# Kernel tuning notes

Measured on AMD Instinct MI355X. Metric: run time of the kernel, lower is better.

Reference implementation:

```python
import jax, jax.numpy as jnp
import numpy as np

B, L, H, D, M = 4, 2048, 16, 64, 128
EPS = 1e-6


def _create_projection_matrix(key, m, d):
    nb_full_blocks = m // d
    keys = jax.random.split(key, nb_full_blocks + 2)
    blocks = []
    for i in range(nb_full_blocks):
        unstructured = jax.random.normal(keys[i], (d, d), dtype=jnp.float32)
        q, _ = jnp.linalg.qr(unstructured)
        blocks.append(q.T)
    remaining = m - nb_full_blocks * d
    if remaining > 0:
        unstructured = jax.random.normal(keys[nb_full_blocks], (d, d), dtype=jnp.float32)
        q, _ = jnp.linalg.qr(unstructured)
        blocks.append(q.T[:remaining])
    final = jnp.concatenate(blocks, axis=0)  # [m, d]
    multiplier = jnp.linalg.norm(jax.random.normal(keys[-1], (m, d), dtype=jnp.float32), axis=1)
    return multiplier[:, None] * final


def setup_inputs() -> dict:
    key = jax.random.key(0)
    kq, kk, kv, kp = jax.random.split(key, 4)
    return {
        "q": jax.random.normal(kq, (B, L, H, D), dtype=jnp.float32),
        "k": jax.random.normal(kk, (B, L, H, D), dtype=jnp.float32),
        "v": jax.random.normal(kv, (B, L, H, D), dtype=jnp.float32),
        "projection_matrix": _create_projection_matrix(kp, M, D),
    }


def _softmax_kernel(data, proj, is_query, eps=EPS):
    # data: [B,L,H,D], proj: [M,D]
    data = (data.shape[-1] ** -0.25) * data
    ratio = proj.shape[0] ** -0.5
    data_dash = jnp.einsum('blhd,md->blhm', data, proj)  # [B,L,H,M]
    diag = jnp.sum(data * data, axis=-1, keepdims=True) * 0.5  # [B,L,H,1]
    if is_query:
        mx = jnp.max(data_dash, axis=-1, keepdims=True)
    else:
        mx = jnp.max(data_dash, axis=(1, 3), keepdims=True)
    return ratio * (jnp.exp(data_dash - diag - mx) + eps)


def reference(q, k, v, projection_matrix):
    qp = _softmax_kernel(q, projection_matrix, True)   # [B,L,H,M]
    kp = _softmax_kernel(k, projection_matrix, False)  # [B,L,H,M]
    # move L to the front for the causal scan
    qs = jnp.swapaxes(qp, 0, 1)  # [L,B,H,M]
    ks = jnp.swapaxes(kp, 0, 1)  # [L,B,H,M]
    vs = jnp.swapaxes(v, 0, 1)   # [L,B,H,D]

    def step(carry, inp):
        s, dsum = carry                 # s: [B,H,M,D], dsum: [B,H,M]
        q_t, k_t, v_t = inp
        s = s + k_t[..., :, None] * v_t[..., None, :]  # outer product accumulate
        dsum = dsum + k_t
        num = jnp.einsum('bhmd,bhm->bhd', s, q_t)      # [B,H,D]
        den = jnp.einsum('bhm,bhm->bh', q_t, dsum)     # [B,H]
        return (s, dsum), (num, den)

    init = (jnp.zeros((qs.shape[1], qs.shape[2], qs.shape[3], vs.shape[3]), qs.dtype),
            jnp.zeros_like(ks[0]))
    _, (nums, dens) = jax.lax.scan(step, init, (qs, ks, vs))
    av = jnp.swapaxes(nums, 0, 1)          # [B,L,H,D]
    norm = jnp.swapaxes(dens, 0, 1)[..., None]  # [B,L,H,1]
    return av / norm
```

## Files before the change

### kernel.cpp

```cpp
#include <hip/hip_runtime.h>
#include <math.h>

#define B_ 4
#define L_ 2048
#define H_ 16
#define D_ 64
#define M_ 128
#define TC_ 64
#define NC_ (L_ / TC_)
#define EPSK 1e-6f
#define DATA_SCALE 0.35355339059327379f
#define RATIO 0.08838834764831845f

typedef __bf16 bf16;
typedef bf16 bf16x4 __attribute__((ext_vector_type(4)));
typedef bf16 bf16x8 __attribute__((ext_vector_type(8)));
typedef float floatx4 __attribute__((ext_vector_type(4)));

#define PK64 72
#define FS_ 136

__device__ __forceinline__ unsigned pk(bf16 a, bf16 b) {
    return (unsigned)__builtin_bit_cast(unsigned short, a) |
           ((unsigned)__builtin_bit_cast(unsigned short, b) << 16);
}

__device__ __forceinline__ unsigned enc_f(float f) {
    unsigned u = __float_as_uint(f);
    return (u & 0x80000000u) ? ~u : (u | 0x80000000u);
}
__device__ __forceinline__ float dec_f(unsigned u) {
    unsigned b = (u & 0x80000000u) ? (u ^ 0x80000000u) : ~u;
    return __uint_as_float(b);
}

__global__ __launch_bounds__(256) void proj_split(const float* __restrict__ proj,
                                                  bf16* __restrict__ pfh,
                                                  bf16* __restrict__ pfl,
                                                  unsigned* __restrict__ mx) {
    int f = blockIdx.x * 256 + threadIdx.x;
    if (blockIdx.x == 0 && threadIdx.x < B_ * H_) mx[threadIdx.x] = 0u;
    int tc = f >> 7, k0h = (f >> 6) & 1, lane = f & 63;
    int lr = lane & 15, quad = lane >> 4;
    const float* src = proj + (16 * tc + lr) * 64 + k0h * 32 + quad * 8;
    float4 x0 = *(const float4*)src;
    float4 x1 = *(const float4*)(src + 4);
    float a[8] = {x0.x, x0.y, x0.z, x0.w, x1.x, x1.y, x1.z, x1.w};
    bf16x8 hi, lo;
#pragma unroll
    for (int e = 0; e < 8; e++) {
        bf16 h = (bf16)a[e];
        hi[e] = h;
        lo[e] = (bf16)(a[e] - (float)h);
    }
    *(bf16x8*)(pfh + (size_t)f * 8) = hi;
    *(bf16x8*)(pfl + (size_t)f * 8) = lo;
}

__global__ __launch_bounds__(256) void feat_max(const float* __restrict__ k,
                                                const bf16* __restrict__ pfh,
                                                unsigned* __restrict__ mxk) {
    __shared__ float wred[4];
    int tid = threadIdx.x;
    int blk = blockIdx.x;
    int c = blk & 31, h = (blk >> 5) & 15, b = blk >> 9;
    int l0 = c * 64;
    int w = tid >> 6, lane = tid & 63, lr = lane & 15, quad = lane >> 4;

    const float* drow = k +
        ((size_t)(b * L_ + l0 + 16 * w + lr) * H_ + h) * D_ + quad * 8;
    bf16x8 ah[2];
#pragma unroll
    for (int k0 = 0; k0 < 2; k0++) {
        float4 x0 = *(const float4*)(drow + k0 * 32);
        float4 x1 = *(const float4*)(drow + k0 * 32 + 4);
        float a[8] = {x0.x, x0.y, x0.z, x0.w, x1.x, x1.y, x1.z, x1.w};
#pragma unroll
        for (int e = 0; e < 8; e++) ah[k0][e] = (bf16)(DATA_SCALE * a[e]);
    }

    floatx4 acc[8];
#pragma unroll
    for (int tc = 0; tc < 8; tc++) acc[tc] = (floatx4){0.f, 0.f, 0.f, 0.f};
    const bf16x8* ph = (const bf16x8*)pfh + lane;
#pragma unroll
    for (int tc = 0; tc < 8; tc++)
#pragma unroll
        for (int k0 = 0; k0 < 2; k0++) {
            bf16x8 bh = ph[(tc * 2 + k0) * 64];
            acc[tc] = __builtin_amdgcn_mfma_f32_16x16x32_bf16(ah[k0], bh, acc[tc], 0, 0, 0);
        }

    float mm = acc[0][0];
#pragma unroll
    for (int tc = 0; tc < 8; tc++)
#pragma unroll
        for (int reg = 0; reg < 4; reg++) mm = fmaxf(mm, acc[tc][reg]);
#pragma unroll
    for (int off = 1; off < 64; off <<= 1) mm = fmaxf(mm, __shfl_xor(mm, off, 64));
    if (lane == 0) wred[w] = mm;
    __syncthreads();
    if (tid == 0) {
        float g = fmaxf(fmaxf(wred[0], wred[1]), fmaxf(wred[2], wred[3]));
        atomicMax(&mxk[b * H_ + h], enc_f(g));
    }
}

__global__ __launch_bounds__(256) void feat_k(const float* __restrict__ kin,
                                              const bf16* __restrict__ pfh,
                                              const bf16* __restrict__ pfl,
                                              const unsigned* __restrict__ mxk,
                                              bf16* __restrict__ kp) {
    __shared__ __align__(16) bf16 sc[64 * FS_];
    int tid = threadIdx.x;
    int blk = blockIdx.x;
    int c = blk & 31, h = (blk >> 5) & 15, b = blk >> 9;
    int l0 = c * 64;
    int w = tid >> 6, lane = tid & 63, lr = lane & 15, quad = lane >> 4;

    const float* drow = kin +
        ((size_t)(b * L_ + l0 + 16 * w + lr) * H_ + h) * D_ + quad * 8;
    bf16x8 ah[2], al[2];
    float ss = 0.f;
#pragma unroll
    for (int k0 = 0; k0 < 2; k0++) {
        float4 x0 = *(const float4*)(drow + k0 * 32);
        float4 x1 = *(const float4*)(drow + k0 * 32 + 4);
        float a[8] = {x0.x, x0.y, x0.z, x0.w, x1.x, x1.y, x1.z, x1.w};
#pragma unroll
        for (int e = 0; e < 8; e++) {
            float s = DATA_SCALE * a[e];
            ss += s * s;
            bf16 hh = (bf16)s;
            ah[k0][e] = hh;
            al[k0][e] = (bf16)(s - (float)hh);
        }
    }
    ss += __shfl_xor(ss, 16, 64);
    ss += __shfl_xor(ss, 32, 64);
    float ssrow = 0.5f * ss;

    floatx4 acc[8];
#pragma unroll
    for (int tc = 0; tc < 8; tc++) acc[tc] = (floatx4){0.f, 0.f, 0.f, 0.f};
    const bf16x8* ph = (const bf16x8*)pfh + lane;
    const bf16x8* pl = (const bf16x8*)pfl + lane;
#pragma unroll
    for (int tc = 0; tc < 8; tc++)
#pragma unroll
        for (int k0 = 0; k0 < 2; k0++) {
            bf16x8 bh = ph[(tc * 2 + k0) * 64];
            bf16x8 bl = pl[(tc * 2 + k0) * 64];
            acc[tc] = __builtin_amdgcn_mfma_f32_16x16x32_bf16(ah[k0], bh, acc[tc], 0, 0, 0);
            acc[tc] = __builtin_amdgcn_mfma_f32_16x16x32_bf16(al[k0], bh, acc[tc], 0, 0, 0);
            acc[tc] = __builtin_amdgcn_mfma_f32_16x16x32_bf16(ah[k0], bl, acc[tc], 0, 0, 0);
        }

    int t0 = 16 * w + 4 * quad;
    float mxg = dec_f(mxk[b * H_ + h]);
#pragma unroll
    for (int reg = 0; reg < 4; reg++) {
        float dg = __shfl(ssrow, 4 * quad + reg, 64);
        float sh = dg + mxg;
#pragma unroll
        for (int tc = 0; tc < 8; tc++) {
            float val = RATIO * (__expf(acc[tc][reg] - sh) + EPSK);
            sc[(t0 + reg) * FS_ + 16 * tc + lr] = (bf16)val;
        }
    }

    {
        uint4* kout = (uint4*)(kp + (size_t)blk * 8192);
#pragma unroll
        for (int ki = 0; ki < 4; ki++)
            kout[(ki * 4 + w) * 64 + lane] =
                *(const uint4*)(sc + (16 * w + lr) * FS_ + 32 * ki + 8 * quad);
    }
}

__global__ __launch_bounds__(256) void chunk_v(const bf16* __restrict__ kp,
                                               const float* __restrict__ v,
                                               bf16* __restrict__ S,
                                               float* __restrict__ ds,
                                               bf16* __restrict__ vbT) {
    __shared__ __align__(16) bf16 kT[128 * PK64];
    __shared__ __align__(16) bf16 vT[64 * PK64];
    int tid = threadIdx.x;
    int blk = blockIdx.x;
    int c = blk & 31, bh = blk >> 5;
    int h = bh & 15, b = bh >> 4;
    int l0 = c * 64;
    int w = tid >> 6, lane = tid & 63, lr = lane & 15, quad = lane >> 4;

    const bf16* kpt = kp + (size_t)blk * 8192;
#pragma unroll
    for (int i = 0; i < 4; i++) {
        int m8 = w * 4 + i;
        bf16x8 kv = *(const bf16x8*)(kpt +
            (((m8 >> 2) * 4 + (lane >> 4)) * 64 + (m8 & 3) * 16 + (lane & 15)) * 8);
#pragma unroll
        for (int e = 0; e < 8; e++) kT[(m8 * 8 + e) * PK64 + lane] = kv[e];
    }
    {
        const float* vrow = v + ((size_t)(b * L_ + l0 + lane) * H_ + h) * D_;
#pragma unroll
        for (int i = 0; i < 4; i++) {
            int d4 = w * 4 + i;
            float4 x = *(const float4*)(vrow + d4 * 4);
            vT[(d4 * 4 + 0) * PK64 + lane] = (bf16)x.x;
            vT[(d4 * 4 + 1) * PK64 + lane] = (bf16)x.y;
            vT[(d4 * 4 + 2) * PK64 + lane] = (bf16)x.z;
            vT[(d4 * 4 + 3) * PK64 + lane] = (bf16)x.w;
        }
    }
    __syncthreads();

    floatx4 acc[8];
#pragma unroll
    for (int tc = 0; tc < 8; tc++) acc[tc] = (floatx4){0.f, 0.f, 0.f, 0.f};
#pragma unroll
    for (int k0 = 0; k0 < 64; k0 += 32) {
        bf16x8 a = *(const bf16x8*)(vT + (16 * w + lr) * PK64 + k0 + quad * 8);
#pragma unroll
        for (int tc = 0; tc < 8; tc++) {
            bf16x8 bb = *(const bf16x8*)(kT + (16 * tc + lr) * PK64 + k0 + quad * 8);
            acc[tc] = __builtin_amdgcn_mfma_f32_16x16x32_bf16(a, bb, acc[tc], 0, 0, 0);
        }
    }

    {
        size_t ob = (size_t)(bh * D_) * (size_t)L_ + l0;
#pragma unroll
        for (int i = 0; i < 8; i++) {
            int e2 = tid + 256 * i;
            int d = e2 >> 5, tau2 = (e2 & 31) * 2;
            *(unsigned*)(vbT + ob + (size_t)d * L_ + tau2) =
                *(const unsigned*)(vT + d * PK64 + tau2);
        }
    }

    float dsv = 0.f;
    {
        int m = tid >> 1, half = tid & 1;
        const bf16x8* kr = (const bf16x8*)(kT + m * PK64 + half * 32);
#pragma unroll
        for (int j = 0; j < 4; j++) {
            bf16x8 vv = kr[j];
#pragma unroll
            for (int e = 0; e < 8; e++) dsv += (float)vv[e];
        }
        dsv += __shfl_xor(dsv, 1, 64);
    }
    __syncthreads();

    bf16* scr = kT;
#pragma unroll
    for (int tc = 0; tc < 8; tc++)
#pragma unroll
        for (int reg = 0; reg < 4; reg++)
            scr[((tc >> 1) * 4 + w) * 512 +
                (((((tc & 1) << 1) | (lr >> 3)) * 16) + 4 * quad + reg) * 8 +
                (lr & 7)] = (bf16)acc[tc][reg];
    if ((tid & 1) == 0) ds[(size_t)blk * M_ + (tid >> 1)] = dsv;
    __syncthreads();
#pragma unroll
    for (int i = 0; i < 4; i++) {
        int e = tid + 256 * i;
        ((uint4*)S)[(size_t)blk * 1024 + e] = ((const uint4*)scr)[e];
    }
}

__global__ void prefix_SD(unsigned* __restrict__ S, float* __restrict__ ds) {
    int blk = blockIdx.x;
    int seg = blk & 15, bh = blk >> 4;
    int p = seg * 256 + threadIdx.x;
    size_t base = (size_t)bh * NC_ * 4096 + p;
    unsigned uv[NC_];
#pragma unroll
    for (int c = 0; c < NC_; c++) uv[c] = S[base + (size_t)c * 4096];
    float c0 = 0.f, c1 = 0.f;
#pragma unroll
    for (int c = 0; c < NC_; c++) {
        unsigned u = uv[c];
        float f0 = (float)__builtin_bit_cast(bf16, (unsigned short)(u & 0xffffu));
        float f1 = (float)__builtin_bit_cast(bf16, (unsigned short)(u >> 16));
        S[base + (size_t)c * 4096] = pk((bf16)c0, (bf16)c1);
        c0 += f0; c1 += f1;
    }
    if (seg == 0 && threadIdx.x < 128) {
        int m = threadIdx.x;
        size_t dbase = (size_t)bh * NC_ * M_ + m;
        float dv[NC_];
#pragma unroll
        for (int c = 0; c < NC_; c++) dv[c] = ds[dbase + (size_t)c * M_];
        float carry = 0.f;
#pragma unroll
        for (int c = 0; c < NC_; c++) {
            ds[dbase + (size_t)c * M_] = carry;
            carry += dv[c];
        }
    }
}

__global__ __launch_bounds__(256, 4) void attn_q(const float* __restrict__ q,
                                                 const bf16* __restrict__ pfh,
                                                 const bf16* __restrict__ pfl,
                                                 const bf16* __restrict__ kp,
                                                 const bf16* __restrict__ vbT,
                                                 const bf16* __restrict__ Sp,
                                                 const float* __restrict__ dp,
                                                 float* __restrict__ out) {
    __shared__ __align__(16) bf16 fsc[64 * FS_];

    int tid = threadIdx.x;
    int blk = blockIdx.x;
    int c = blk & 31, bh = blk >> 5;
    int h = bh & 15, b = bh >> 4;
    int l0 = c * 64;
    int w = tid >> 6, lane = tid & 63, lr = lane & 15, quad = lane >> 4;

    const float* drow = q +
        ((size_t)(b * L_ + l0 + 16 * w + lr) * H_ + h) * D_ + quad * 8;
    bf16x8 ah[2], al[2];
    float ss = 0.f;
#pragma unroll
    for (int k0 = 0; k0 < 2; k0++) {
        float4 x0 = *(const float4*)(drow + k0 * 32);
        float4 x1 = *(const float4*)(drow + k0 * 32 + 4);
        float a[8] = {x0.x, x0.y, x0.z, x0.w, x1.x, x1.y, x1.z, x1.w};
#pragma unroll
        for (int e = 0; e < 8; e++) {
            float s = DATA_SCALE * a[e];
            ss += s * s;
            bf16 hh = (bf16)s;
            ah[k0][e] = hh;
            al[k0][e] = (bf16)(s - (float)hh);
        }
    }
    ss += __shfl_xor(ss, 16, 64);
    ss += __shfl_xor(ss, 32, 64);
    float ssrow = 0.5f * ss;

    floatx4 facc[8];
#pragma unroll
    for (int tc = 0; tc < 8; tc++) facc[tc] = (floatx4){0.f, 0.f, 0.f, 0.f};
    {
        const bf16x8* ph = (const bf16x8*)pfh + lane;
        const bf16x8* pl = (const bf16x8*)pfl + lane;
#pragma unroll
        for (int tc = 0; tc < 8; tc++)
#pragma unroll
            for (int k0 = 0; k0 < 2; k0++) {
                bf16x8 bh = ph[(tc * 2 + k0) * 64];
                bf16x8 bl = pl[(tc * 2 + k0) * 64];
                facc[tc] = __builtin_amdgcn_mfma_f32_16x16x32_bf16(ah[k0], bh, facc[tc], 0, 0, 0);
                facc[tc] = __builtin_amdgcn_mfma_f32_16x16x32_bf16(al[k0], bh, facc[tc], 0, 0, 0);
                facc[tc] = __builtin_amdgcn_mfma_f32_16x16x32_bf16(ah[k0], bl, facc[tc], 0, 0, 0);
            }
    }
    int t0 = 16 * w + 4 * quad;
#pragma unroll
    for (int reg = 0; reg < 4; reg++) {
        float m = facc[0][reg];
#pragma unroll
        for (int tc = 1; tc < 8; tc++) m = fmaxf(m, facc[tc][reg]);
        m = fmaxf(m, __shfl_xor(m, 1, 64));
        m = fmaxf(m, __shfl_xor(m, 2, 64));
        m = fmaxf(m, __shfl_xor(m, 4, 64));
        m = fmaxf(m, __shfl_xor(m, 8, 64));
        float dg = __shfl(ssrow, 4 * quad + reg, 64);
        float sh = dg + m;
#pragma unroll
        for (int tc = 0; tc < 8; tc++) {
            float val = RATIO * (__expf(facc[tc][reg] - sh) + EPSK);
            fsc[(t0 + reg) * FS_ + 16 * tc + lr] = (bf16)val;
        }
    }

    bf16x8 af[4];
#pragma unroll
    for (int k = 0; k < 4; k++)
        af[k] = *(const bf16x8*)(fsc + (16 * w + lr) * FS_ + 32 * k + quad * 8);

    floatx4 acc[4];
#pragma unroll
    for (int tc = 0; tc < 4; tc++) acc[tc] = (floatx4){0.f, 0.f, 0.f, 0.f};

    {
        const bf16x8* spb = (const bf16x8*)(Sp + (size_t)blk * 8192) + lane;
        bf16x8 sp4[16];
#pragma unroll
        for (int f = 0; f < 16; f++) sp4[f] = spb[f * 64];
#pragma unroll
        for (int ki = 0; ki < 4; ki++)
#pragma unroll
            for (int tc = 0; tc < 4; tc++)
                acc[tc] = __builtin_amdgcn_mfma_f32_16x16x32_bf16(af[ki], sp4[ki * 4 + tc],
                                                                  acc[tc], 0, 0, 0);
    }

    floatx4 acc2[4];
#pragma unroll
    for (int tc = 0; tc < 4; tc++) acc2[tc] = (floatx4){0.f, 0.f, 0.f, 0.f};
    {
        const bf16x8* kpb = (const bf16x8*)(kp + (size_t)blk * 8192) + lane;
        bf16x8 kb[16];
#pragma unroll
        for (int f = 0; f < 16; f++) kb[f] = kpb[f * 64];
#pragma unroll
        for (int ki = 0; ki < 4; ki++)
#pragma unroll
            for (int tc = 0; tc < 4; tc++)
                if (tc <= w)
                    acc2[tc] = __builtin_amdgcn_mfma_f32_16x16x32_bf16(af[ki], kb[ki * 4 + tc],
                                                                       acc2[tc], 0, 0, 0);
    }

    float densc[4];
    {
        float dsum[4] = {0.f, 0.f, 0.f, 0.f};
#pragma unroll
        for (int tc = 0; tc < 4; tc++) {
#pragma unroll
            for (int reg = 0; reg < 4; reg++) {
                int tg = t0 + reg, tau = 16 * tc + lr;
                float vv = (tc <= w) ? acc2[tc][reg] : 0.f;
                if (tau > tg) vv = 0.f;
                dsum[reg] += vv;
                fsc[tg * FS_ + tau] = (bf16)vv;
            }
        }
#pragma unroll
        for (int reg = 0; reg < 4; reg++) {
            float s = dsum[reg];
            s += __shfl_xor(s, 1, 64);
            s += __shfl_xor(s, 2, 64);
            s += __shfl_xor(s, 4, 64);
            s += __shfl_xor(s, 8, 64);
            densc[reg] = s;
        }
    }

    float den0v = 0.f;
    {
        const float* dpb = dp + (size_t)blk * M_ + quad * 8;
#pragma unroll
        for (int k = 0; k < 4; k++) {
            float4 d0 = *(const float4*)(dpb + 32 * k);
            float4 d1 = *(const float4*)(dpb + 32 * k + 4);
            den0v += (float)af[k][0] * d0.x + (float)af[k][1] * d0.y +
                     (float)af[k][2] * d0.z + (float)af[k][3] * d0.w +
                     (float)af[k][4] * d1.x + (float)af[k][5] * d1.y +
                     (float)af[k][6] * d1.z + (float)af[k][7] * d1.w;
        }
    }
    den0v += __shfl_xor(den0v, 16, 64);
    den0v += __shfl_xor(den0v, 32, 64);

    {
        const bf16* vbb = vbT + (size_t)(bh * D_) * L_ + l0 + quad * 8;
        int kmax = (w >= 2) ? 64 : 32;
        for (int k0 = 0; k0 < kmax; k0 += 32) {
            bf16x8 a = *(const bf16x8*)(fsc + (16 * w + lr) * FS_ + k0 + quad * 8);
#pragma unroll
            for (int tc = 0; tc < 4; tc++) {
                bf16x8 bb = *(const bf16x8*)(vbb + (size_t)(16 * tc + lr) * L_ + k0);
                acc[tc] = __builtin_amdgcn_mfma_f32_16x16x32_bf16(a, bb, acc[tc], 0, 0, 0);
            }
        }
    }

    {
        float inv[4];
#pragma unroll
        for (int reg = 0; reg < 4; reg++) {
            float d0 = __shfl(den0v, 4 * quad + reg, 64);
            inv[reg] = 1.0f / (d0 + densc[reg]);
        }
#pragma unroll
        for (int tc = 0; tc < 4; tc++)
#pragma unroll
            for (int reg = 0; reg < 4; reg++)
                out[((size_t)(b * L_ + l0 + t0 + reg) * H_ + h) * D_ + 16 * tc + lr] =
                    acc[tc][reg] * inv[reg];
    }
}

extern "C" void kernel_launch(void* const* d_in, const int* in_sizes, int n_in,
                              void* d_out, int out_size, void* d_ws, size_t ws_size,
                              hipStream_t stream) {
    const float* q = (const float*)d_in[0];
    const float* k = (const float*)d_in[1];
    const float* v = (const float*)d_in[2];
    const float* proj = (const float*)d_in[3];
    float* out = (float*)d_out;
    char* W = (char*)d_ws;

    bf16* kp   = (bf16*)(W);
    bf16* vbT  = (bf16*)(W + 33554432ull);
    bf16* S    = (bf16*)(W + 50331648ull);
    float* ds  = (float*)(W + 83886080ull);
    unsigned* mx = (unsigned*)(W + 84934656ull);
    bf16* pfh  = (bf16*)(W + 84934912ull);
    bf16* pfl  = (bf16*)(W + 84951296ull);

    hipLaunchKernelGGL(proj_split, dim3(4), dim3(256), 0, stream, proj, pfh, pfl, mx);
    hipLaunchKernelGGL(feat_max, dim3(2048), dim3(256), 0, stream, k, pfh, mx);
    hipLaunchKernelGGL(feat_k, dim3(2048), dim3(256), 0, stream, k, pfh, pfl, mx, kp);
    hipLaunchKernelGGL(chunk_v, dim3(2048), dim3(256), 0, stream, kp, v, S, ds, vbT);
    hipLaunchKernelGGL(prefix_SD, dim3(1024), dim3(256), 0, stream, (unsigned*)S, ds);
    hipLaunchKernelGGL(attn_q, dim3(2048), dim3(256), 0, stream,
                       q, pfh, pfl, kp, vbT, S, ds, out);
}
```

Before: 223.7 us.

## Split feature and attention kernels into single-wave blocks with causal kb load skip

feat_max, feat_k and attn_q now launch one 64-thread wave per 16-row slice instead of four waves per 64-row chunk, so there are four times as many blocks, each with a quarter of the shared memory. No wave waits on a block barrier and blocks can be scheduled more freely. The shared-memory wmax reduction becomes one atomicMax per wave, which multiplies atomic traffic by four. attn_q also skips loading key-feature fragments that the causal mask would zero, at the cost of more redundant global reads of shared S/kp tiles across blocks.

After: 287.9 us. +28.7%, slower.

```diff
diff --git a/kernel.cpp b/kernel.cpp
--- a/kernel.cpp
+++ b/kernel.cpp
@@ -57,15 +57,13 @@
     *(bf16x8*)(pfl + (size_t)f * 8) = lo;
 }
 
-__global__ __launch_bounds__(256) void feat_max(const float* __restrict__ k,
-                                                const bf16* __restrict__ pfh,
-                                                unsigned* __restrict__ mxk) {
-    __shared__ float wred[4];
-    int tid = threadIdx.x;
+__global__ __launch_bounds__(64, 4) void feat_max(const float* __restrict__ k,
+                                                  const bf16* __restrict__ pfh,
+                                                  unsigned* __restrict__ mxk) {
     int blk = blockIdx.x;
-    int c = blk & 31, h = (blk >> 5) & 15, b = blk >> 9;
+    int w = blk & 3, c = (blk >> 2) & 31, h = (blk >> 7) & 15, b = blk >> 11;
     int l0 = c * 64;
-    int w = tid >> 6, lane = tid & 63, lr = lane & 15, quad = lane >> 4;
+    int lane = threadIdx.x, lr = lane & 15, quad = lane >> 4;
 
     const float* drow = k +
         ((size_t)(b * L_ + l0 + 16 * w + lr) * H_ + h) * D_ + quad * 8;
@@ -98,25 +96,20 @@
         for (int reg = 0; reg < 4; reg++) mm = fmaxf(mm, acc[tc][reg]);
 #pragma unroll
     for (int off = 1; off < 64; off <<= 1) mm = fmaxf(mm, __shfl_xor(mm, off, 64));
-    if (lane == 0) wred[w] = mm;
-    __syncthreads();
-    if (tid == 0) {
-        float g = fmaxf(fmaxf(wred[0], wred[1]), fmaxf(wred[2], wred[3]));
-        atomicMax(&mxk[b * H_ + h], enc_f(g));
-    }
-}
-
-__global__ __launch_bounds__(256) void feat_k(const float* __restrict__ kin,
-                                              const bf16* __restrict__ pfh,
-                                              const bf16* __restrict__ pfl,
-                                              const unsigned* __restrict__ mxk,
-                                              bf16* __restrict__ kp) {
-    __shared__ __align__(16) bf16 sc[64 * FS_];
-    int tid = threadIdx.x;
+    if (lane == 0) atomicMax(&mxk[b * H_ + h], enc_f(mm));
+}
+
+__global__ __launch_bounds__(64, 4) void feat_k(const float* __restrict__ kin,
+                                                const bf16* __restrict__ pfh,
+                                                const bf16* __restrict__ pfl,
+                                                const unsigned* __restrict__ mxk,
+                                                bf16* __restrict__ kp) {
+    __shared__ __align__(16) bf16 sc[16 * FS_];
     int blk = blockIdx.x;
-    int c = blk & 31, h = (blk >> 5) & 15, b = blk >> 9;
+    int w = blk & 3, c = (blk >> 2) & 31, h = (blk >> 7) & 15, b = blk >> 11;
     int l0 = c * 64;
-    int w = tid >> 6, lane = tid & 63, lr = lane & 15, quad = lane >> 4;
+    int lane = threadIdx.x, lr = lane & 15, quad = lane >> 4;
+    int tile = (blk >> 2);
 
     const float* drow = kin +
         ((size_t)(b * L_ + l0 + 16 * w + lr) * H_ + h) * D_ + quad * 8;
@@ -156,7 +149,6 @@
             acc[tc] = __builtin_amdgcn_mfma_f32_16x16x32_bf16(ah[k0], bl, acc[tc], 0, 0, 0);
         }
 
-    int t0 = 16 * w + 4 * quad;
     float mxg = dec_f(mxk[b * H_ + h]);
 #pragma unroll
     for (int reg = 0; reg < 4; reg++) {
@@ -165,16 +157,16 @@
 #pragma unroll
         for (int tc = 0; tc < 8; tc++) {
             float val = RATIO * (__expf(acc[tc][reg] - sh) + EPSK);
-            sc[(t0 + reg) * FS_ + 16 * tc + lr] = (bf16)val;
-        }
-    }
-
-    {
-        uint4* kout = (uint4*)(kp + (size_t)blk * 8192);
+            sc[(4 * quad + reg) * FS_ + 16 * tc + lr] = (bf16)val;
+        }
+    }
+
+    {
+        uint4* kout = (uint4*)(kp + (size_t)tile * 8192);
 #pragma unroll
         for (int ki = 0; ki < 4; ki++)
             kout[(ki * 4 + w) * 64 + lane] =
-                *(const uint4*)(sc + (16 * w + lr) * FS_ + 32 * ki + 8 * quad);
+                *(const uint4*)(sc + lr * FS_ + 32 * ki + 8 * quad);
     }
 }
 
@@ -302,22 +294,22 @@
     }
 }
 
-__global__ __launch_bounds__(256, 4) void attn_q(const float* __restrict__ q,
-                                                 const bf16* __restrict__ pfh,
-                                                 const bf16* __restrict__ pfl,
-                                                 const bf16* __restrict__ kp,
-                                                 const bf16* __restrict__ vbT,
-                                                 const bf16* __restrict__ Sp,
-                                                 const float* __restrict__ dp,
-                                                 float* __restrict__ out) {
-    __shared__ __align__(16) bf16 fsc[64 * FS_];
-
-    int tid = threadIdx.x;
+__global__ __launch_bounds__(64, 4) void attn_q(const float* __restrict__ q,
+                                                const bf16* __restrict__ pfh,
+                                                const bf16* __restrict__ pfl,
+                                                const bf16* __restrict__ kp,
+                                                const bf16* __restrict__ vbT,
+                                                const bf16* __restrict__ Sp,
+                                                const float* __restrict__ dp,
+                                                float* __restrict__ out) {
+    __shared__ __align__(16) bf16 fsc[16 * FS_];
+
     int blk = blockIdx.x;
-    int c = blk & 31, bh = blk >> 5;
+    int w = blk & 3, c = (blk >> 2) & 31, bh = blk >> 7;
     int h = bh & 15, b = bh >> 4;
     int l0 = c * 64;
-    int w = tid >> 6, lane = tid & 63, lr = lane & 15, quad = lane >> 4;
+    int tile = blk >> 2;
+    int lane = threadIdx.x, lr = lane & 15, quad = lane >> 4;
 
     const float* drow = q +
         ((size_t)(b * L_ + l0 + 16 * w + lr) * H_ + h) * D_ + quad * 8;
@@ -358,7 +350,6 @@
                 facc[tc] = __builtin_amdgcn_mfma_f32_16x16x32_bf16(ah[k0], bl, facc[tc], 0, 0, 0);
             }
     }
-    int t0 = 16 * w + 4 * quad;
 #pragma unroll
     for (int reg = 0; reg < 4; reg++) {
         float m = facc[0][reg];
@@ -373,21 +364,21 @@
 #pragma unroll
         for (int tc = 0; tc < 8; tc++) {
             float val = RATIO * (__expf(facc[tc][reg] - sh) + EPSK);
-            fsc[(t0 + reg) * FS_ + 16 * tc + lr] = (bf16)val;
+            fsc[(4 * quad + reg) * FS_ + 16 * tc + lr] = (bf16)val;
         }
     }
 
     bf16x8 af[4];
 #pragma unroll
     for (int k = 0; k < 4; k++)
-        af[k] = *(const bf16x8*)(fsc + (16 * w + lr) * FS_ + 32 * k + quad * 8);
+        af[k] = *(const bf16x8*)(fsc + lr * FS_ + 32 * k + quad * 8);
 
     floatx4 acc[4];
 #pragma unroll
     for (int tc = 0; tc < 4; tc++) acc[tc] = (floatx4){0.f, 0.f, 0.f, 0.f};
 
     {
-        const bf16x8* spb = (const bf16x8*)(Sp + (size_t)blk * 8192) + lane;
+        const bf16x8* spb = (const bf16x8*)(Sp + (size_t)tile * 8192) + lane;
         bf16x8 sp4[16];
 #pragma unroll
         for (int f = 0; f < 16; f++) sp4[f] = spb[f * 64];
@@ -403,10 +394,13 @@
 #pragma unroll
     for (int tc = 0; tc < 4; tc++) acc2[tc] = (floatx4){0.f, 0.f, 0.f, 0.f};
     {
-        const bf16x8* kpb = (const bf16x8*)(kp + (size_t)blk * 8192) + lane;
+        const bf16x8* kpb = (const bf16x8*)(kp + (size_t)tile * 8192) + lane;
         bf16x8 kb[16];
 #pragma unroll
-        for (int f = 0; f < 16; f++) kb[f] = kpb[f * 64];
+        for (int ki = 0; ki < 4; ki++)
+#pragma unroll
+            for (int tc = 0; tc < 4; tc++)
+                if (tc <= w) kb[ki * 4 + tc] = kpb[(ki * 4 + tc) * 64];
 #pragma unroll
         for (int ki = 0; ki < 4; ki++)
 #pragma unroll
@@ -423,11 +417,11 @@
         for (int tc = 0; tc < 4; tc++) {
 #pragma unroll
             for (int reg = 0; reg < 4; reg++) {
-                int tg = t0 + reg, tau = 16 * tc + lr;
+                int tg = 16 * w + 4 * quad + reg, tau = 16 * tc + lr;
                 float vv = (tc <= w) ? acc2[tc][reg] : 0.f;
                 if (tau > tg) vv = 0.f;
                 dsum[reg] += vv;
-                fsc[tg * FS_ + tau] = (bf16)vv;
+                fsc[(4 * quad + reg) * FS_ + tau] = (bf16)vv;
             }
         }
 #pragma unroll
@@ -443,7 +437,7 @@
 
     float den0v = 0.f;
     {
-        const float* dpb = dp + (size_t)blk * M_ + quad * 8;
+        const float* dpb = dp + (size_t)tile * M_ + quad * 8;
 #pragma unroll
         for (int k = 0; k < 4; k++) {
             float4 d0 = *(const float4*)(dpb + 32 * k);
@@ -459,13 +453,16 @@
 
     {
         const bf16* vbb = vbT + (size_t)(bh * D_) * L_ + l0 + quad * 8;
-        int kmax = (w >= 2) ? 64 : 32;
-        for (int k0 = 0; k0 < kmax; k0 += 32) {
-            bf16x8 a = *(const bf16x8*)(fsc + (16 * w + lr) * FS_ + k0 + quad * 8);
-#pragma unroll
-            for (int tc = 0; tc < 4; tc++) {
-                bf16x8 bb = *(const bf16x8*)(vbb + (size_t)(16 * tc + lr) * L_ + k0);
-                acc[tc] = __builtin_amdgcn_mfma_f32_16x16x32_bf16(a, bb, acc[tc], 0, 0, 0);
+#pragma unroll
+        for (int k0i = 0; k0i < 2; k0i++) {
+            if (k0i == 0 || w >= 2) {
+                int k0 = k0i * 32;
+                bf16x8 a = *(const bf16x8*)(fsc + lr * FS_ + k0 + quad * 8);
+#pragma unroll
+                for (int tc = 0; tc < 4; tc++) {
+                    bf16x8 bb = *(const bf16x8*)(vbb + (size_t)(16 * tc + lr) * L_ + k0);
+                    acc[tc] = __builtin_amdgcn_mfma_f32_16x16x32_bf16(a, bb, acc[tc], 0, 0, 0);
+                }
             }
         }
     }
@@ -481,8 +478,8 @@
         for (int tc = 0; tc < 4; tc++)
 #pragma unroll
             for (int reg = 0; reg < 4; reg++)
-                out[((size_t)(b * L_ + l0 + t0 + reg) * H_ + h) * D_ + 16 * tc + lr] =
-                    acc[tc][reg] * inv[reg];
+                out[((size_t)(b * L_ + l0 + 16 * w + 4 * quad + reg) * H_ + h) * D_ +
+                    16 * tc + lr] = acc[tc][reg] * inv[reg];
     }
 }
 
@@ -505,10 +502,10 @@
     bf16* pfl  = (bf16*)(W + 84951296ull);
 
     hipLaunchKernelGGL(proj_split, dim3(4), dim3(256), 0, stream, proj, pfh, pfl, mx);
-    hipLaunchKernelGGL(feat_max, dim3(2048), dim3(256), 0, stream, k, pfh, mx);
-    hipLaunchKernelGGL(feat_k, dim3(2048), dim3(256), 0, stream, k, pfh, pfl, mx, kp);
+    hipLaunchKernelGGL(feat_max, dim3(8192), dim3(64), 0, stream, k, pfh, mx);
+    hipLaunchKernelGGL(feat_k, dim3(8192), dim3(64), 0, stream, k, pfh, pfl, mx, kp);
     hipLaunchKernelGGL(chunk_v, dim3(2048), dim3(256), 0, stream, kp, v, S, ds, vbT);
     hipLaunchKernelGGL(prefix_SD, dim3(1024), dim3(256), 0, stream, (unsigned*)S, ds);
-    hipLaunchKernelGGL(attn_q, dim3(2048), dim3(256), 0, stream,
+    hipLaunchKernelGGL(attn_q, dim3(8192), dim3(64), 0, stream,
                        q, pfh, pfl, kp, vbT, S, ds, out);
 }
```
